# Performance work log

Measured on AMD Instinct MI355X. Metric: run time of the kernel, lower is better.

## Reference

```python
import jax, jax.numpy as jnp
import numpy as np
from jax import lax

GAMMA = 1.0
INF = 1000000.0  # matches the TF code's pseudo-infinity


def _pairwise_sq_dists(a, b):
    # ||a_i - b_j||^2 = ||a||^2 + ||b||^2 - 2 a.b ; avoids the [B,N,M,d] diff tensor
    a2 = jnp.sum(a * a, axis=-1)                      # (B, N)
    b2 = jnp.sum(b * b, axis=-1)                      # (B, M)
    ab = jnp.einsum('bnd,bmd->bnm', a, b)             # (B, N, M)
    return a2[:, :, None] + b2[:, None, :] - 2.0 * ab


def _soft_dtw(seq_a, seq_b, gamma):
    D = _pairwise_sq_dists(seq_a, seq_b)              # (B, N, M)
    B, N, M = D.shape
    dtype = D.dtype
    # row 0 of the DP table: R[0,0]=0, R[0,j>0]=INF
    row0 = jnp.full((B, M + 1), INF, dtype=dtype).at[:, 0].set(0.0)

    def row_step(prev_row, d_i):
        # prev_row: (B, M+1) = R[i-1, :]; d_i: (B, M) = D[:, i-1, :]
        def col_step(left, inputs):
            diag, up, d = inputs                      # each (B,)
            r = jnp.stack([diag, up, left], axis=-1)  # (B, 3)
            softmin = -gamma * jax.nn.logsumexp(-r / gamma, axis=-1)
            val = d + softmin
            return val, val
        left0 = jnp.full((B,), INF, dtype=dtype)      # R[i, 0] = INF
        xs = (prev_row[:, :-1].T, prev_row[:, 1:].T, d_i.T)  # scan over M
        _, vals = lax.scan(col_step, left0, xs)       # (M, B)
        new_row = jnp.concatenate([jnp.full((B, 1), INF, dtype=dtype), vals.T], axis=1)
        return new_row, None

    final_row, _ = lax.scan(row_step, row0, jnp.moveaxis(D, 1, 0))
    return final_row[:, -1]                           # R[N, M]


def setup_inputs() -> dict:
    key = jax.random.key(0)
    k1, k2 = jax.random.split(key)
    B, N, M, d = 128, 384, 384, 128
    seq_a = jax.random.normal(k1, (B, N, d), dtype=jnp.float32)
    seq_b = jax.random.normal(k2, (B, M, d), dtype=jnp.float32)
    return {"seq_a": seq_a, "seq_b": seq_b}


def reference(seq_a, seq_b):
    dist = _soft_dtw(seq_a, seq_b, GAMMA)
    return dist[:, None]                              # (B, 1)
```

## Files before the change

### kernel.cpp

```cpp
#include <hip/hip_runtime.h>
#include <stdint.h>

#define BATCH 128
#define SEQN  384
#define SEQM  384
#define DIM   128
#define KINF   1000000.0f
#define LOG2E  1.4426950408889634f
#define LN2    0.6931471805599453f
#define KINF2  (KINF * LOG2E)

#define RING    204
#define RSTRIDE 392
#define NCHUNK  13

#define EXP2F(x) __builtin_amdgcn_exp2f(x)
#define LOG2F(x) __builtin_amdgcn_logf(x)

typedef __attribute__((ext_vector_type(8))) short bf16x8;
typedef __attribute__((ext_vector_type(4))) float f32x4;

__device__ __forceinline__ unsigned short bf16_rne(float x) {
    uint32_t u = __float_as_uint(x);
    u += 0x7FFFu + ((u >> 16) & 1u);
    return (unsigned short)(u >> 16);
}
__device__ __forceinline__ uint32_t bf16_pair(float x, float y) {
    uint32_t ux = __float_as_uint(x); ux += 0x7FFFu + ((ux >> 16) & 1u);
    uint32_t uy = __float_as_uint(y); uy += 0x7FFFu + ((uy >> 16) & 1u);
    return (ux >> 16) | (uy & 0xFFFF0000u);
}

union frag_u { bf16x8 v; uint32_t u[4]; };

__global__ __launch_bounds__(256) void fused_dtw(
        const float* __restrict__ A, const float* __restrict__ B,
        float* __restrict__ out) {
    __shared__ __align__(16) unsigned short ring[RING * RSTRIDE];
    __shared__ __align__(16) float normA[SEQN];
    __shared__ int prod_done[16];
    __shared__ int cons_pp;

    const int bat  = blockIdx.x;
    const int tid  = threadIdx.x;
    const int wv   = tid >> 6;
    const int lane = tid & 63;

    if (tid < 16) prod_done[tid] = 0;
    if (tid == 16) cons_pp = -1;
    __syncthreads();

    if (wv != 0) {
        const int l16 = lane & 15, q = lane >> 4;
        const int sbase = (wv - 1) * 8;
        const float* __restrict__ Ab = A + (long)bat * SEQN * DIM;
        const float* __restrict__ Bb = B + (long)bat * SEQM * DIM;
        bool first = true;
        for (int k = 0; k < NCHUNK; k++) {
            if (k >= 6) {
                int thr = 8 * k - 12, g = 0;
                while (__hip_atomic_load(&cons_pp, __ATOMIC_ACQUIRE,
                                         __HIP_MEMORY_SCOPE_WORKGROUP) < thr)
                    if (++g > (1 << 22)) break;
            }
            if (k == 12) {
                if (wv == 1) {
                    uint32_t pv = bf16_pair(KINF2, KINF2);
                    #pragma unroll
                    for (int c = 0; c < 4; c++) {
                        uint32_t* p = (uint32_t*)&ring[(384 - RING + c) * RSTRIDE + 6 * lane];
                        p[0] = pv; p[1] = pv; p[2] = pv;
                    }
                }
            } else {
                frag_u bfrag[2][4];
                float bn[2];
                #pragma unroll
                for (int jg = 0; jg < 2; jg++) {
                    const float* bp = Bb + (long)(32 * k + jg * 16 + l16) * DIM + q * 8;
                    float s = 0.0f;
                    #pragma unroll
                    for (int kk = 0; kk < 4; kk++) {
                        float4 v0 = *(const float4*)(bp + kk * 32);
                        float4 v1 = *(const float4*)(bp + kk * 32 + 4);
                        bfrag[jg][kk].u[0] = bf16_pair(v0.x, v0.y);
                        bfrag[jg][kk].u[1] = bf16_pair(v0.z, v0.w);
                        bfrag[jg][kk].u[2] = bf16_pair(v1.x, v1.y);
                        bfrag[jg][kk].u[3] = bf16_pair(v1.z, v1.w);
                        s += v0.x*v0.x + v0.y*v0.y + v0.z*v0.z + v0.w*v0.w
                           + v1.x*v1.x + v1.y*v1.y + v1.z*v1.z + v1.w*v1.w;
                    }
                    s += __shfl_xor(s, 16, 64);
                    s += __shfl_xor(s, 32, 64);
                    bn[jg] = s;
                }
                float4 c0v[4], c1v[4];
                {
                    const float* ap = Ab + (long)(sbase * 16 + l16) * DIM + q * 8;
                    #pragma unroll
                    for (int kk = 0; kk < 4; kk++) {
                        c0v[kk] = *(const float4*)(ap + kk * 32);
                        c1v[kk] = *(const float4*)(ap + kk * 32 + 4);
                    }
                }
                #pragma unroll
                for (int s8 = 0; s8 < 8; s8++) {
                    const int si = sbase + s8;
                    float4 n0[4], n1[4];
                    if (s8 < 7) {
                        const float* ap = Ab + (long)((si + 1) * 16 + l16) * DIM + q * 8;
                        #pragma unroll
                        for (int kk = 0; kk < 4; kk++) {
                            n0[kk] = *(const float4*)(ap + kk * 32);
                            n1[kk] = *(const float4*)(ap + kk * 32 + 4);
                        }
                    }
                    frag_u afr[4];
                    #pragma unroll
                    for (int kk = 0; kk < 4; kk++) {
                        afr[kk].u[0] = bf16_pair(c0v[kk].x, c0v[kk].y);
                        afr[kk].u[1] = bf16_pair(c0v[kk].z, c0v[kk].w);
                        afr[kk].u[2] = bf16_pair(c1v[kk].x, c1v[kk].y);
                        afr[kk].u[3] = bf16_pair(c1v[kk].z, c1v[kk].w);
                    }
                    if (first) {
                        float sa = 0.0f;
                        #pragma unroll
                        for (int kk = 0; kk < 4; kk++)
                            sa += c0v[kk].x*c0v[kk].x + c0v[kk].y*c0v[kk].y
                                + c0v[kk].z*c0v[kk].z + c0v[kk].w*c0v[kk].w
                                + c1v[kk].x*c1v[kk].x + c1v[kk].y*c1v[kk].y
                                + c1v[kk].z*c1v[kk].z + c1v[kk].w*c1v[kk].w;
                        sa += __shfl_xor(sa, 16, 64);
                        sa += __shfl_xor(sa, 32, 64);
                        if (q == 0) normA[si * 16 + l16] = sa;
                    }
                    f32x4 acc0 = {0.0f, 0.0f, 0.0f, 0.0f};
                    f32x4 acc1 = {0.0f, 0.0f, 0.0f, 0.0f};
                    #pragma unroll
                    for (int kk = 0; kk < 4; kk++) {
                        acc0 = __builtin_amdgcn_mfma_f32_16x16x32_bf16(
                                   afr[kk].v, bfrag[0][kk].v, acc0, 0, 0, 0);
                        acc1 = __builtin_amdgcn_mfma_f32_16x16x32_bf16(
                                   afr[kk].v, bfrag[1][kk].v, acc1, 0, 0, 0);
                    }
                    if (first) asm volatile("s_waitcnt lgkmcnt(0)" ::: "memory");
                    float4 an = *(const float4*)&normA[si * 16 + q * 4];
                    #pragma unroll
                    for (int jg = 0; jg < 2; jg++) {
                        int col  = 32 * k + jg * 16 + l16;
                        int slot = col >= RING ? col - RING : col;
                        f32x4 ac = jg ? acc1 : acc0;
                        ushort4 pk;
                        pk.x = bf16_rne((an.x + bn[jg] - 2.0f * ac[0]) * LOG2E);
                        pk.y = bf16_rne((an.y + bn[jg] - 2.0f * ac[1]) * LOG2E);
                        pk.z = bf16_rne((an.z + bn[jg] - 2.0f * ac[2]) * LOG2E);
                        pk.w = bf16_rne((an.w + bn[jg] - 2.0f * ac[3]) * LOG2E);
                        *(ushort4*)&ring[slot * RSTRIDE + si * 16 + q * 4] = pk;
                    }
                    if (s8 < 7) {
                        #pragma unroll
                        for (int kk = 0; kk < 4; kk++) { c0v[kk] = n0[kk]; c1v[kk] = n1[kk]; }
                    }
                }
                first = false;
            }
            __hip_atomic_fetch_add(&prod_done[k], 1, __ATOMIC_RELEASE,
                                   __HIP_MEMORY_SCOPE_WORKGROUP);
        }
        return;
    }

    const int t = lane;
    {
        int g = 0;
        while (__hip_atomic_load(&prod_done[0], __ATOMIC_ACQUIRE,
                                 __HIP_MEMORY_SCOPE_WORKGROUP) < 3)
            if (++g > (1 << 22)) break;
    }
    const unsigned short* __restrict__ ringT = ring + 6 * t;

    float prev[6];
    #pragma unroll
    for (int r = 0; r < 6; r++) prev[r] = KINF2;

    uint3 dslot[4];
    #pragma unroll
    for (int qq = 0; qq < 4; qq++) {
        int c = qq - 2 * t;
        int cc = c < 0 ? 0 : c;
        dslot[qq] = *(const uint3*)(ringT + cc * RSTRIDE);
    }

    float rcv0 = KINF2, rcv1 = KINF2, old_diag = KINF2;
    float lane0_diag = 0.0f;
    const bool isl0 = (t == 0);
    int c0 = -2 * t;

#define UNPACK(d, w)                                                        \
    d[0] = __uint_as_float(w.x << 16);                                      \
    d[1] = __uint_as_float(w.x & 0xFFFF0000u);                              \
    d[2] = __uint_as_float(w.y << 16);                                      \
    d[3] = __uint_as_float(w.y & 0xFFFF0000u);                              \
    d[4] = __uint_as_float(w.z << 16);                                      \
    d[5] = __uint_as_float(w.z & 0xFFFF0000u);

#define COLPASS(dX, diag0, upseed, LEFTV, NEWV)                             \
    {                                                                       \
        float Bp = (upseed), Fp = 1.0f;                                     \
        float Bv[6], Fv[6];                                                 \
        _Pragma("unroll")                                                   \
        for (int r = 0; r < 6; r++) {                                       \
            float vd = (r == 0) ? (diag0) : LEFTV[r - 1];                   \
            float vl = LEFTV[r];                                            \
            float m3 = fminf(fminf(vd, vl), Bp);            \
            float al = EXP2F(m3 - Bp);                                      \
            float be = EXP2F(m3 - vd) + EXP2F(m3 - vl);                     \
            float Fr = __builtin_fmaf(al, Fp, be);                          \
            float Br = dX[r] + m3;                                          \
            Bv[r] = Br; Fv[r] = Fr;                                         \
            Bp = Br; Fp = Fr;                                               \
        }                                                                   \
        _Pragma("unroll")                                                   \
        for (int r = 0; r < 6; r++)                                         \
            NEWV[r] = Bv[r] - LOG2F(Fv[r]);                                 \
    }

#define PHASE2(Q)                                                           \
    {                                                                       \
        uint3 wA = dslot[Q];                                                \
        uint3 wB = dslot[(Q) + 1];                                          \
        {            \
            int cnA = c0 + 4;                                               \
            int ccA = cnA < 0 ? 0 : (cnA > 387 ? 387 : cnA);                \
            int sA  = ccA >= RING ? ccA - RING : ccA;                       \
            int cnB = c0 + 5;                                               \
            int ccB = cnB < 0 ? 0 : (cnB > 387 ? 387 : cnB);                \
            int sB  = ccB >= RING ? ccB - RING : ccB;                       \
            dslot[Q]       = *(const uint3*)(ringT + sA * RSTRIDE);         \
            dslot[(Q) + 1] = *(const uint3*)(ringT + sB * RSTRIDE);         \
        }                                                                   \
        float dA[6], dB[6];                                                 \
        UNPACK(dA, wA)                                                      \
        UNPACK(dB, wB)                                                      \
        float dgA = isl0 ? lane0_diag : old_diag;                           \
        float upA = isl0 ? KINF2 : rcv0;                                    \
        float upB = isl0 ? KINF2 : rcv1;                                    \
        float newA[6];                                                      \
        COLPASS(dA, dgA, upA, prev, newA)                                   \
        COLPASS(dB, upA, upB, newA, prev)                                   \
        old_diag = rcv1;                                                    \
        rcv0 = __shfl_up(newA[5], 1, 64);                                   \
        rcv1 = __shfl_up(prev[5], 1, 64);                                   \
        lane0_diag = KINF2;                                                 \
        c0 += 2;                                                            \
    }

    for (int pp = 0; pp < 127; pp++) {
        if ((pp & 7) == 7) {
            int k = (4 * pp + 7) >> 5;
            if (k < NCHUNK) {
                int g = 0;
                while (__hip_atomic_load(&prod_done[k], __ATOMIC_ACQUIRE,
                                         __HIP_MEMORY_SCOPE_WORKGROUP) < 3)
                    if (++g > (1 << 22)) break;
            }
        }
        PHASE2(0)
        PHASE2(2)
        if (t == 0)
            __hip_atomic_store(&cons_pp, pp,
                               __ATOMIC_RELEASE, __HIP_MEMORY_SCOPE_WORKGROUP);
    }
    PHASE2(0)
#undef PHASE2
#undef COLPASS
#undef UNPACK

    if (t == 63) out[bat] = prev[5] * LN2;
}

extern "C" void kernel_launch(void* const* d_in, const int* in_sizes, int n_in,
                              void* d_out, int out_size, void* d_ws, size_t ws_size,
                              hipStream_t stream) {
    (void)in_sizes; (void)n_in; (void)out_size; (void)d_ws; (void)ws_size;
    const float* a = (const float*)d_in[0];
    const float* b = (const float*)d_in[1];
    float* out = (float*)d_out;

    fused_dtw<<<dim3(BATCH), dim3(256), 0, stream>>>(a, b, out);
}
```

Before: 195.1 us.

## Carry DP values as (base, mantissa) pairs to drop per-cell log2

Each DP cell is now kept as a pair (B, F) holding the exponent offset and a mantissa in [1,2), normalised with bit manipulation. This replaces the per-cell LOG2F on the consumer's critical path, and a single log is taken at the output. It costs an extra multiply per neighbour, twice the register state, and twice the cross-lane shuffles per phase. The producer's completion atomic is also limited to one lane, cutting redundant atomic traffic.

Result: slower. 215.4 us (+10.4%).

```diff
diff --git a/kernel.cpp b/kernel.cpp
--- a/kernel.cpp
+++ b/kernel.cpp
@@ -165,8 +165,9 @@
                 }
                 first = false;
             }
-            __hip_atomic_fetch_add(&prod_done[k], 1, __ATOMIC_RELEASE,
-                                   __HIP_MEMORY_SCOPE_WORKGROUP);
+            if (lane == 0)
+                __hip_atomic_fetch_add(&prod_done[k], 1, __ATOMIC_RELEASE,
+                                       __HIP_MEMORY_SCOPE_WORKGROUP);
         }
         return;
     }
@@ -180,20 +181,22 @@
     }
     const unsigned short* __restrict__ ringT = ring + 6 * t;
 
-    float prev[6];
+    float prevB[6], prevF[6];
     #pragma unroll
-    for (int r = 0; r < 6; r++) prev[r] = KINF2;
+    for (int r = 0; r < 6; r++) { prevB[r] = KINF2; prevF[r] = 1.0f; }
 
     uint3 dslot[4];
     #pragma unroll
     for (int qq = 0; qq < 4; qq++) {
         int c = qq - 2 * t;
         int cc = c < 0 ? 0 : c;
-        dslot[qq] = *(const uint3*)(ringT + cc * RSTRIDE);
-    }
-
-    float rcv0 = KINF2, rcv1 = KINF2, old_diag = KINF2;
-    float lane0_diag = 0.0f;
+        dslot[qq] = *(const uint3*)(ringT + (long)cc * RSTRIDE);
+    }
+
+    float rcv0B = KINF2, rcv0F = 1.0f;
+    float rcv1B = KINF2, rcv1F = 1.0f;
+    float odB   = KINF2, odF   = 1.0f;
+    float l0dB  = 0.0f,  l0dF  = 1.0f;
     const bool isl0 = (t == 0);
     int c0 = -2 * t;
 
@@ -205,25 +208,25 @@
     d[4] = __uint_as_float(w.z << 16);                                      \
     d[5] = __uint_as_float(w.z & 0xFFFF0000u);
 
-#define COLPASS(dX, diag0, upseed, LEFTV, NEWV)                             \
+#define COLPASS(dX, dgB_, dgF_, upB_, upF_, LB, LF, NB, NF)                 \
     {                                                                       \
-        float Bp = (upseed), Fp = 1.0f;                                     \
-        float Bv[6], Fv[6];                                                 \
+        float Bp = (upB_), Fp = (upF_);                                     \
         _Pragma("unroll")                                                   \
         for (int r = 0; r < 6; r++) {                                       \
-            float vd = (r == 0) ? (diag0) : LEFTV[r - 1];                   \
-            float vl = LEFTV[r];                                            \
-            float m3 = fminf(fminf(vd, vl), Bp);            \
-            float al = EXP2F(m3 - Bp);                                      \
-            float be = EXP2F(m3 - vd) + EXP2F(m3 - vl);                     \
-            float Fr = __builtin_fmaf(al, Fp, be);                          \
+            float vdB = (r == 0) ? (dgB_) : LB[r - 1];                      \
+            float vdF = (r == 0) ? (dgF_) : LF[r - 1];                      \
+            float vlB = LB[r], vlF = LF[r];                                 \
+            float m3 = fminf(fminf(vdB, vlB), Bp);          \
+            float Fr = EXP2F(m3 - Bp) * Fp;                                 \
+            Fr = __builtin_fmaf(EXP2F(m3 - vdB), vdF, Fr);                  \
+            Fr = __builtin_fmaf(EXP2F(m3 - vlB), vlF, Fr);                  \
             float Br = dX[r] + m3;                                          \
-            Bv[r] = Br; Fv[r] = Fr;                                         \
-            Bp = Br; Fp = Fr;                                               \
+            uint32_t fb = __float_as_uint(Fr);                              \
+            int e = (int)(fb >> 23) - 127;                                  \
+            NB[r] = Br - (float)e;                                          \
+            NF[r] = __uint_as_float((fb & 0x007FFFFFu) | 0x3F800000u);      \
+            Bp = Br; Fp = Fr;           \
         }                                                                   \
-        _Pragma("unroll")                                                   \
-        for (int r = 0; r < 6; r++)                                         \
-            NEWV[r] = Bv[r] - LOG2F(Fv[r]);                                 \
     }
 
 #define PHASE2(Q)                                                           \
@@ -237,22 +240,27 @@
             int cnB = c0 + 5;                                               \
             int ccB = cnB < 0 ? 0 : (cnB > 387 ? 387 : cnB);                \
             int sB  = ccB >= RING ? ccB - RING : ccB;                       \
-            dslot[Q]       = *(const uint3*)(ringT + sA * RSTRIDE);         \
-            dslot[(Q) + 1] = *(const uint3*)(ringT + sB * RSTRIDE);         \
+            dslot[Q]       = *(const uint3*)(ringT + (long)sA * RSTRIDE);   \
+            dslot[(Q) + 1] = *(const uint3*)(ringT + (long)sB * RSTRIDE);   \
         }                                                                   \
-        float dA[6], dB[6];                                                 \
+        float dA[6], dB6[6];                                                \
         UNPACK(dA, wA)                                                      \
-        UNPACK(dB, wB)                                                      \
-        float dgA = isl0 ? lane0_diag : old_diag;                           \
-        float upA = isl0 ? KINF2 : rcv0;                                    \
-        float upB = isl0 ? KINF2 : rcv1;                                    \
-        float newA[6];                                                      \
-        COLPASS(dA, dgA, upA, prev, newA)                                   \
-        COLPASS(dB, upA, upB, newA, prev)                                   \
-        old_diag = rcv1;                                                    \
-        rcv0 = __shfl_up(newA[5], 1, 64);                                   \
-        rcv1 = __shfl_up(prev[5], 1, 64);                                   \
-        lane0_diag = KINF2;                                                 \
+        UNPACK(dB6, wB)                                                     \
+        float dgAB = isl0 ? l0dB : odB;                                     \
+        float dgAF = isl0 ? l0dF : odF;                                     \
+        float upAB = isl0 ? KINF2 : rcv0B;                                  \
+        float upAF = isl0 ? 1.0f  : rcv0F;                                  \
+        float upBB = isl0 ? KINF2 : rcv1B;                                  \
+        float upBF = isl0 ? 1.0f  : rcv1F;                                  \
+        float nAB[6], nAF[6];                                               \
+        COLPASS(dA,  dgAB, dgAF, upAB, upAF, prevB, prevF, nAB, nAF)        \
+        COLPASS(dB6, upAB, upAF, upBB, upBF, nAB, nAF, prevB, prevF)        \
+        odB = rcv1B; odF = rcv1F;                                           \
+        rcv0B = __shfl_up(nAB[5],   1, 64);                                 \
+        rcv0F = __shfl_up(nAF[5],   1, 64);                                 \
+        rcv1B = __shfl_up(prevB[5], 1, 64);                                 \
+        rcv1F = __shfl_up(prevF[5], 1, 64);                                 \
+        l0dB = KINF2; l0dF = 1.0f;                                          \
         c0 += 2;                                                            \
     }
 
@@ -277,7 +285,7 @@
 #undef COLPASS
 #undef UNPACK
 
-    if (t == 63) out[bat] = prev[5] * LN2;
+    if (t == 63) out[bat] = (prevB[5] - LOG2F(prevF[5])) * LN2;
 }
 
 extern "C" void kernel_launch(void* const* d_in, const int* in_sizes, int n_in,
```

## Double producer waves, add dedicated INF-padding wave, raise consumer priority

Applied to the files above, without the earlier changes.

The block grows from 256 to 512 threads. Six producer waves now each compute 4 row-strips of the distance tile instead of three waves doing 8, and a separate wave writes the INF padding columns once the consumer reaches a set point. The single consumer wave raises its scheduling priority, and producers sleep while spin-waiting so they take fewer issue slots from it. The aim is to keep the serial DP wavefront from stalling on distance production, at the cost of more waves contending for the CU and extra synchronisation counts.

Result: slower. 199.1 us (+2.0%).

```diff
diff --git a/kernel.cpp b/kernel.cpp
--- a/kernel.cpp
+++ b/kernel.cpp
@@ -12,10 +12,11 @@
 
 #define RING    204
 #define RSTRIDE 392
-#define NCHUNK  13
 
 #define EXP2F(x) __builtin_amdgcn_exp2f(x)
 #define LOG2F(x) __builtin_amdgcn_logf(x)
+
+#define WG __HIP_MEMORY_SCOPE_WORKGROUP
 
 typedef __attribute__((ext_vector_type(8))) short bf16x8;
 typedef __attribute__((ext_vector_type(4))) float f32x4;
@@ -33,7 +34,7 @@
 
 union frag_u { bf16x8 v; uint32_t u[4]; };
 
-__global__ __launch_bounds__(256) void fused_dtw(
+__global__ __launch_bounds__(512) void fused_dtw(
         const float* __restrict__ A, const float* __restrict__ B,
         float* __restrict__ out) {
     __shared__ __align__(16) unsigned short ring[RING * RSTRIDE];
@@ -50,123 +51,131 @@
     if (tid == 16) cons_pp = -1;
     __syncthreads();
 
+    if (wv == 4) {
+        int g = 0;
+        while (__hip_atomic_load(&cons_pp, __ATOMIC_ACQUIRE, WG) < 84) {
+            __builtin_amdgcn_s_sleep(8);
+            if (++g > (1 << 20)) break;
+        }
+        uint32_t pv = bf16_pair(KINF2, KINF2);
+        #pragma unroll
+        for (int c = 0; c < 4; c++) {
+            uint32_t* p = (uint32_t*)&ring[(384 - RING + c) * RSTRIDE + 6 * lane];
+            p[0] = pv; p[1] = pv; p[2] = pv;
+        }
+        if (lane == 0)
+            __hip_atomic_fetch_add(&prod_done[12], 6, __ATOMIC_RELEASE, WG);
+        return;
+    }
+
     if (wv != 0) {
+        const int pidx  = (wv < 4) ? (wv - 1) : (wv - 2);
+        const int sbase = pidx * 4;
         const int l16 = lane & 15, q = lane >> 4;
-        const int sbase = (wv - 1) * 8;
         const float* __restrict__ Ab = A + (long)bat * SEQN * DIM;
         const float* __restrict__ Bb = B + (long)bat * SEQM * DIM;
         bool first = true;
-        for (int k = 0; k < NCHUNK; k++) {
+        for (int k = 0; k < 12; k++) {
             if (k >= 6) {
                 int thr = 8 * k - 12, g = 0;
-                while (__hip_atomic_load(&cons_pp, __ATOMIC_ACQUIRE,
-                                         __HIP_MEMORY_SCOPE_WORKGROUP) < thr)
-                    if (++g > (1 << 22)) break;
-            }
-            if (k == 12) {
-                if (wv == 1) {
-                    uint32_t pv = bf16_pair(KINF2, KINF2);
-                    #pragma unroll
-                    for (int c = 0; c < 4; c++) {
-                        uint32_t* p = (uint32_t*)&ring[(384 - RING + c) * RSTRIDE + 6 * lane];
-                        p[0] = pv; p[1] = pv; p[2] = pv;
-                    }
-                }
-            } else {
-                frag_u bfrag[2][4];
-                float bn[2];
-                #pragma unroll
-                for (int jg = 0; jg < 2; jg++) {
-                    const float* bp = Bb + (long)(32 * k + jg * 16 + l16) * DIM + q * 8;
-                    float s = 0.0f;
+                while (__hip_atomic_load(&cons_pp, __ATOMIC_ACQUIRE, WG) < thr) {
+                    __builtin_amdgcn_s_sleep(2);
+                    if (++g > (1 << 21)) break;
+                }
+            }
+            frag_u bfrag[2][4];
+            float bn[2];
+            #pragma unroll
+            for (int jg = 0; jg < 2; jg++) {
+                const float* bp = Bb + (long)(32 * k + jg * 16 + l16) * DIM + q * 8;
+                float s = 0.0f;
+                #pragma unroll
+                for (int kk = 0; kk < 4; kk++) {
+                    float4 v0 = *(const float4*)(bp + kk * 32);
+                    float4 v1 = *(const float4*)(bp + kk * 32 + 4);
+                    bfrag[jg][kk].u[0] = bf16_pair(v0.x, v0.y);
+                    bfrag[jg][kk].u[1] = bf16_pair(v0.z, v0.w);
+                    bfrag[jg][kk].u[2] = bf16_pair(v1.x, v1.y);
+                    bfrag[jg][kk].u[3] = bf16_pair(v1.z, v1.w);
+                    s += v0.x*v0.x + v0.y*v0.y + v0.z*v0.z + v0.w*v0.w
+                       + v1.x*v1.x + v1.y*v1.y + v1.z*v1.z + v1.w*v1.w;
+                }
+                s += __shfl_xor(s, 16, 64);
+                s += __shfl_xor(s, 32, 64);
+                bn[jg] = s;
+            }
+            float4 c0v[4], c1v[4];
+            {
+                const float* ap = Ab + (long)(sbase * 16 + l16) * DIM + q * 8;
+                #pragma unroll
+                for (int kk = 0; kk < 4; kk++) {
+                    c0v[kk] = *(const float4*)(ap + kk * 32);
+                    c1v[kk] = *(const float4*)(ap + kk * 32 + 4);
+                }
+            }
+            #pragma unroll
+            for (int s4 = 0; s4 < 4; s4++) {
+                const int si = sbase + s4;
+                float4 n0[4], n1[4];
+                if (s4 < 3) {
+                    const float* ap = Ab + (long)((si + 1) * 16 + l16) * DIM + q * 8;
                     #pragma unroll
                     for (int kk = 0; kk < 4; kk++) {
-                        float4 v0 = *(const float4*)(bp + kk * 32);
-                        float4 v1 = *(const float4*)(bp + kk * 32 + 4);
-                        bfrag[jg][kk].u[0] = bf16_pair(v0.x, v0.y);
-                        bfrag[jg][kk].u[1] = bf16_pair(v0.z, v0.w);
-                        bfrag[jg][kk].u[2] = bf16_pair(v1.x, v1.y);
-                        bfrag[jg][kk].u[3] = bf16_pair(v1.z, v1.w);
-                        s += v0.x*v0.x + v0.y*v0.y + v0.z*v0.z + v0.w*v0.w
-                           + v1.x*v1.x + v1.y*v1.y + v1.z*v1.z + v1.w*v1.w;
+                        n0[kk] = *(const float4*)(ap + kk * 32);
+                        n1[kk] = *(const float4*)(ap + kk * 32 + 4);
                     }
-                    s += __shfl_xor(s, 16, 64);
-                    s += __shfl_xor(s, 32, 64);
-                    bn[jg] = s;
-                }
-                float4 c0v[4], c1v[4];
-                {
-                    const float* ap = Ab + (long)(sbase * 16 + l16) * DIM + q * 8;
+                }
+                frag_u afr[4];
+                #pragma unroll
+                for (int kk = 0; kk < 4; kk++) {
+                    afr[kk].u[0] = bf16_pair(c0v[kk].x, c0v[kk].y);
+                    afr[kk].u[1] = bf16_pair(c0v[kk].z, c0v[kk].w);
+                    afr[kk].u[2] = bf16_pair(c1v[kk].x, c1v[kk].y);
+                    afr[kk].u[3] = bf16_pair(c1v[kk].z, c1v[kk].w);
+                }
+                if (first) {
+                    float sa = 0.0f;
                     #pragma unroll
-                    for (int kk = 0; kk < 4; kk++) {
-                        c0v[kk] = *(const float4*)(ap + kk * 32);
-                        c1v[kk] = *(const float4*)(ap + kk * 32 + 4);
-                    }
-                }
-                #pragma unroll
-                for (int s8 = 0; s8 < 8; s8++) {
-                    const int si = sbase + s8;
-                    float4 n0[4], n1[4];
-                    if (s8 < 7) {
-                        const float* ap = Ab + (long)((si + 1) * 16 + l16) * DIM + q * 8;
-                        #pragma unroll
-                        for (int kk = 0; kk < 4; kk++) {
-                            n0[kk] = *(const float4*)(ap + kk * 32);
-                            n1[kk] = *(const float4*)(ap + kk * 32 + 4);
-                        }
-                    }
-                    frag_u afr[4];
+                    for (int kk = 0; kk < 4; kk++)
+                        sa += c0v[kk].x*c0v[kk].x + c0v[kk].y*c0v[kk].y
+                            + c0v[kk].z*c0v[kk].z + c0v[kk].w*c0v[kk].w
+                            + c1v[kk].x*c1v[kk].x + c1v[kk].y*c1v[kk].y
+                            + c1v[kk].z*c1v[kk].z + c1v[kk].w*c1v[kk].w;
+                    sa += __shfl_xor(sa, 16, 64);
+                    sa += __shfl_xor(sa, 32, 64);
+                    if (q == 0) normA[si * 16 + l16] = sa;
+                }
+                f32x4 acc0 = {0.0f, 0.0f, 0.0f, 0.0f};
+                f32x4 acc1 = {0.0f, 0.0f, 0.0f, 0.0f};
+                #pragma unroll
+                for (int kk = 0; kk < 4; kk++) {
+                    acc0 = __builtin_amdgcn_mfma_f32_16x16x32_bf16(
+                               afr[kk].v, bfrag[0][kk].v, acc0, 0, 0, 0);
+                    acc1 = __builtin_amdgcn_mfma_f32_16x16x32_bf16(
+                               afr[kk].v, bfrag[1][kk].v, acc1, 0, 0, 0);
+                }
+                if (first) asm volatile("s_waitcnt lgkmcnt(0)" ::: "memory");
+                float4 an = *(const float4*)&normA[si * 16 + q * 4];
+                #pragma unroll
+                for (int jg = 0; jg < 2; jg++) {
+                    int col  = 32 * k + jg * 16 + l16;
+                    int slot = col >= RING ? col - RING : col;
+                    f32x4 ac = jg ? acc1 : acc0;
+                    ushort4 pk;
+                    pk.x = bf16_rne((an.x + bn[jg] - 2.0f * ac[0]) * LOG2E);
+                    pk.y = bf16_rne((an.y + bn[jg] - 2.0f * ac[1]) * LOG2E);
+                    pk.z = bf16_rne((an.z + bn[jg] - 2.0f * ac[2]) * LOG2E);
+                    pk.w = bf16_rne((an.w + bn[jg] - 2.0f * ac[3]) * LOG2E);
+                    *(ushort4*)&ring[slot * RSTRIDE + si * 16 + q * 4] = pk;
+                }
+                if (s4 < 3) {
                     #pragma unroll
-                    for (int kk = 0; kk < 4; kk++) {
-                        afr[kk].u[0] = bf16_pair(c0v[kk].x, c0v[kk].y);
-                        afr[kk].u[1] = bf16_pair(c0v[kk].z, c0v[kk].w);
-                        afr[kk].u[2] = bf16_pair(c1v[kk].x, c1v[kk].y);
-                        afr[kk].u[3] = bf16_pair(c1v[kk].z, c1v[kk].w);
-                    }
-                    if (first) {
-                        float sa = 0.0f;
-                        #pragma unroll
-                        for (int kk = 0; kk < 4; kk++)
-                            sa += c0v[kk].x*c0v[kk].x + c0v[kk].y*c0v[kk].y
-                                + c0v[kk].z*c0v[kk].z + c0v[kk].w*c0v[kk].w
-                                + c1v[kk].x*c1v[kk].x + c1v[kk].y*c1v[kk].y
-                                + c1v[kk].z*c1v[kk].z + c1v[kk].w*c1v[kk].w;
-                        sa += __shfl_xor(sa, 16, 64);
-                        sa += __shfl_xor(sa, 32, 64);
-                        if (q == 0) normA[si * 16 + l16] = sa;
-                    }
-                    f32x4 acc0 = {0.0f, 0.0f, 0.0f, 0.0f};
-                    f32x4 acc1 = {0.0f, 0.0f, 0.0f, 0.0f};
-                    #pragma unroll
-                    for (int kk = 0; kk < 4; kk++) {
-                        acc0 = __builtin_amdgcn_mfma_f32_16x16x32_bf16(
-                                   afr[kk].v, bfrag[0][kk].v, acc0, 0, 0, 0);
-                        acc1 = __builtin_amdgcn_mfma_f32_16x16x32_bf16(
-                                   afr[kk].v, bfrag[1][kk].v, acc1, 0, 0, 0);
-                    }
-                    if (first) asm volatile("s_waitcnt lgkmcnt(0)" ::: "memory");
-                    float4 an = *(const float4*)&normA[si * 16 + q * 4];
-                    #pragma unroll
-                    for (int jg = 0; jg < 2; jg++) {
-                        int col  = 32 * k + jg * 16 + l16;
-                        int slot = col >= RING ? col - RING : col;
-                        f32x4 ac = jg ? acc1 : acc0;
-                        ushort4 pk;
-                        pk.x = bf16_rne((an.x + bn[jg] - 2.0f * ac[0]) * LOG2E);
-                        pk.y = bf16_rne((an.y + bn[jg] - 2.0f * ac[1]) * LOG2E);
-                        pk.z = bf16_rne((an.z + bn[jg] - 2.0f * ac[2]) * LOG2E);
-                        pk.w = bf16_rne((an.w + bn[jg] - 2.0f * ac[3]) * LOG2E);
-                        *(ushort4*)&ring[slot * RSTRIDE + si * 16 + q * 4] = pk;
-                    }
-                    if (s8 < 7) {
-                        #pragma unroll
-                        for (int kk = 0; kk < 4; kk++) { c0v[kk] = n0[kk]; c1v[kk] = n1[kk]; }
-                    }
-                }
-                first = false;
-            }
-            __hip_atomic_fetch_add(&prod_done[k], 1, __ATOMIC_RELEASE,
-                                   __HIP_MEMORY_SCOPE_WORKGROUP);
+                    for (int kk = 0; kk < 4; kk++) { c0v[kk] = n0[kk]; c1v[kk] = n1[kk]; }
+                }
+            }
+            first = false;
+            if (lane == 0)
+                __hip_atomic_fetch_add(&prod_done[k], 1, __ATOMIC_RELEASE, WG);
         }
         return;
     }
@@ -174,10 +183,10 @@
     const int t = lane;
     {
         int g = 0;
-        while (__hip_atomic_load(&prod_done[0], __ATOMIC_ACQUIRE,
-                                 __HIP_MEMORY_SCOPE_WORKGROUP) < 3)
+        while (__hip_atomic_load(&prod_done[0], __ATOMIC_ACQUIRE, WG) < 6)
             if (++g > (1 << 22)) break;
     }
+    __builtin_amdgcn_s_setprio(1);
     const unsigned short* __restrict__ ringT = ring + 6 * t;
 
     float prev[6];
@@ -189,7 +198,7 @@
     for (int qq = 0; qq < 4; qq++) {
         int c = qq - 2 * t;
         int cc = c < 0 ? 0 : c;
-        dslot[qq] = *(const uint3*)(ringT + cc * RSTRIDE);
+        dslot[qq] = *(const uint3*)(ringT + (long)cc * RSTRIDE);
     }
 
     float rcv0 = KINF2, rcv1 = KINF2, old_diag = KINF2;
@@ -237,8 +246,8 @@
             int cnB = c0 + 5;                                               \
             int ccB = cnB < 0 ? 0 : (cnB > 387 ? 387 : cnB);                \
             int sB  = ccB >= RING ? ccB - RING : ccB;                       \
-            dslot[Q]       = *(const uint3*)(ringT + sA * RSTRIDE);         \
-            dslot[(Q) + 1] = *(const uint3*)(ringT + sB * RSTRIDE);         \
+            dslot[Q]       = *(const uint3*)(ringT + (long)sA * RSTRIDE);   \
+            dslot[(Q) + 1] = *(const uint3*)(ringT + (long)sB * RSTRIDE);   \
         }                                                                   \
         float dA[6], dB[6];                                                 \
         UNPACK(dA, wA)                                                      \
@@ -259,18 +268,16 @@
     for (int pp = 0; pp < 127; pp++) {
         if ((pp & 7) == 7) {
             int k = (4 * pp + 7) >> 5;
-            if (k < NCHUNK) {
+            if (k < 13) {
                 int g = 0;
-                while (__hip_atomic_load(&prod_done[k], __ATOMIC_ACQUIRE,
-                                         __HIP_MEMORY_SCOPE_WORKGROUP) < 3)
+                while (__hip_atomic_load(&prod_done[k], __ATOMIC_ACQUIRE, WG) < 6)
                     if (++g > (1 << 22)) break;
             }
         }
         PHASE2(0)
         PHASE2(2)
         if (t == 0)
-            __hip_atomic_store(&cons_pp, pp,
-                               __ATOMIC_RELEASE, __HIP_MEMORY_SCOPE_WORKGROUP);
+            __hip_atomic_store(&cons_pp, pp, __ATOMIC_RELEASE, WG);
     }
     PHASE2(0)
 #undef PHASE2
@@ -288,5 +295,5 @@
     const float* b = (const float*)d_in[1];
     float* out = (float*)d_out;
 
-    fused_dtw<<<dim3(BATCH), dim3(256), 0, stream>>>(a, b, out);
-}
+    fused_dtw<<<dim3(BATCH), dim3(512), 0, stream>>>(a, b, out);
+}
```
